# Performance work log

Measured on AMD Instinct MI355X. Metric: run time of the kernel, lower is better.

The kernel has to match this reference:

```python
import jax, jax.numpy as jnp
import numpy as np

EPS = 1e-5

def _conv1x1(x, w):
    # x: (B, Cin, N, K), w: (Cout, Cin) -> (B, Cout, N, K)
    return jnp.einsum('oc,bcnk->bonk', w, x)

def _bn2d(x, gamma, beta):
    # eval-mode BN with running_mean=0, running_var=1 (fresh init)
    scale = gamma / jnp.sqrt(1.0 + EPS)
    return x * scale[None, :, None, None] + beta[None, :, None, None]

def setup_inputs() -> dict:
    key = jax.random.key(0)
    ks = jax.random.split(key, 10)
    B, Cin, N, K = 8, 64, 1024, 32
    Cout, M = 64, 8
    Cin2 = 2 * Cin  # kernel_input='w_neighbor'
    features = jax.random.normal(ks[0], (B, Cin, N, K), dtype=jnp.float32)
    points_xyz = jax.random.normal(ks[1], (B, 3, N, K), dtype=jnp.float32)
    # ScoreNet convs: mlp_channels [7,16,16,16,M]; first 3 have BN (no bias), last has bias
    w1 = jax.random.normal(ks[2], (16, 7), dtype=jnp.float32) * (2.0 / 7) ** 0.5
    w2 = jax.random.normal(ks[3], (16, 16), dtype=jnp.float32) * (2.0 / 16) ** 0.5
    w3 = jax.random.normal(ks[4], (16, 16), dtype=jnp.float32) * (2.0 / 16) ** 0.5
    w4 = jax.random.normal(ks[5], (M, 16), dtype=jnp.float32) * (2.0 / 16) ** 0.5
    b4 = jnp.zeros((M,), dtype=jnp.float32)
    g1 = jnp.ones((16,), jnp.float32); be1 = jnp.zeros((16,), jnp.float32)
    g2 = jnp.ones((16,), jnp.float32); be2 = jnp.zeros((16,), jnp.float32)
    g3 = jnp.ones((16,), jnp.float32); be3 = jnp.zeros((16,), jnp.float32)
    # weight bank: kaiming_normal on (M, 2Cin, Cout) -> stored as (2Cin, M, Cout)
    wb = jax.random.normal(ks[6], (Cin2, M, Cout), dtype=jnp.float32) * (2.0 / Cin2) ** 0.5
    bn_g = jnp.ones((Cout,), jnp.float32); bn_b = jnp.zeros((Cout,), jnp.float32)
    return dict(features=features, points_xyz=points_xyz,
                w1=w1, g1=g1, be1=be1, w2=w2, g2=g2, be2=be2,
                w3=w3, g3=g3, be3=be3, w4=w4, b4=b4,
                weight_bank=wb, bn_g=bn_g, bn_b=bn_b)

def reference(features, points_xyz, w1, g1, be1, w2, g2, be2, w3, g3, be3,
              w4, b4, weight_bank, bn_g, bn_b):
    B, Cin, N, K = features.shape
    M = weight_bank.shape[1]
    # kernel_input = 'w_neighbor': concat(feat - center, feat) -> (B, 2Cin, N, K)
    center_f = features[..., :1]
    feat = jnp.concatenate([features - center_f, features], axis=1)
    # scorenet input = 'w_neighbor_dist': (center_xyz, xyz_diff, dist) -> (B, 7, N, K)
    center_xyz = jnp.broadcast_to(points_xyz[..., :1], points_xyz.shape)
    xyz_diff = points_xyz - center_xyz
    dist = jnp.sqrt(jnp.sum(xyz_diff * xyz_diff, axis=1, keepdims=True))
    xyz_feats = jnp.concatenate([center_xyz, xyz_diff, dist], axis=1)
    h = jax.nn.relu(_bn2d(_conv1x1(xyz_feats, w1), g1, be1))
    h = jax.nn.relu(_bn2d(_conv1x1(h, w2), g2, be2))
    h = jax.nn.relu(_bn2d(_conv1x1(h, w3), g3, be3))
    s = _conv1x1(h, w4) + b4[None, :, None, None]  # (B, M, N, K)
    scores = jax.nn.softmax(s, axis=1)
    scores = jnp.transpose(scores, (0, 2, 3, 1))  # (B, N, K, M)
    # matmul with weight bank then score-weighted sum over kernels, fused via einsum
    # original: (B,N,K,2Cin)@(2Cin,M*Cout) -> (B,N,K,M,Cout); sum_m scores * . -> (B,N,K,Cout)
    new_features = jnp.einsum('bcnk,cmo,bnkm->bonk', feat, weight_bank, scores)
    # BN2d (eval, fresh stats) + ReLU
    new_features = jax.nn.relu(_bn2d(new_features, bn_g, bn_b))
    return new_features
```

## Files before the change

kernel.cpp:

```cpp
#include <hip/hip_runtime.h>
#include <hip/hip_bf16.h>

typedef _Float16 f16;
typedef __attribute__((ext_vector_type(2))) _Float16 f16x2;
typedef __attribute__((ext_vector_type(8))) _Float16 f16x8;
typedef __attribute__((ext_vector_type(16))) float f32x16;

#define BNSCL 0.9999950000375f

__global__ __launch_bounds__(256) void k_scores(
    const float* __restrict__ xyz,
    const float* __restrict__ w1, const float* __restrict__ g1, const float* __restrict__ be1,
    const float* __restrict__ w2, const float* __restrict__ g2, const float* __restrict__ be2,
    const float* __restrict__ w3, const float* __restrict__ g3, const float* __restrict__ be3,
    const float* __restrict__ w4, const float* __restrict__ b4,
    const float* __restrict__ wb, f16* __restrict__ wbtA,
    f16* __restrict__ scores)
{
    __shared__ float lw[856];
    const int tid = threadIdx.x;

    if (blockIdx.x < 256) {
        int idx = blockIdx.x * 256 + tid;
        int j    = idx & 7;
        int lane = (idx >> 3) & 63;
        int ks   = (idx >> 9) & 63;
        int ot   = idx >> 15;
        int cp   = ks * 2 + (lane >> 5);
        int o    = ot * 32 + (lane & 31);
        wbtA[idx] = (f16)wb[(cp * 8 + j) * 64 + o];
    }

    if (tid < 112) lw[tid] = w1[tid];
    lw[112 + tid] = w2[tid];
    lw[368 + tid] = w3[tid];
    if (tid < 128) lw[624 + tid] = w4[tid];
    if (tid < 8)   lw[752 + tid] = b4[tid];
    if (tid < 16) {
        lw[760 + tid] = g1[tid] * BNSCL;  lw[776 + tid] = be1[tid];
        lw[792 + tid] = g2[tid] * BNSCL;  lw[808 + tid] = be2[tid];
        lw[824 + tid] = g3[tid] * BNSCL;  lw[840 + tid] = be3[tid];
    }
    __syncthreads();

    float in7[2][7], h1[2][16], h2[2][16], s[2][8];

#pragma unroll
    for (int q = 0; q < 2; ++q) {
        int g = blockIdx.x * 512 + q * 256 + tid;
        int b = g >> 15;
        int p = g & 32767;
        int pc = p & ~31;
        const float* xb = xyz + (size_t)b * 98304;
        float cx = xb[pc], cy = xb[32768 + pc], cz = xb[65536 + pc];
        float dx = xb[p] - cx, dy = xb[32768 + p] - cy, dz = xb[65536 + p] - cz;
        in7[q][0] = cx; in7[q][1] = cy; in7[q][2] = cz;
        in7[q][3] = dx; in7[q][4] = dy; in7[q][5] = dz;
        in7[q][6] = sqrtf(dx * dx + dy * dy + dz * dz);
    }

#pragma unroll
    for (int o = 0; o < 16; ++o) {
        float a0 = 0.f, a1 = 0.f;
#pragma unroll
        for (int c = 0; c < 7; ++c) {
            float w = lw[o * 7 + c];
            a0 += w * in7[0][c]; a1 += w * in7[1][c];
        }
        float gs = lw[760 + o], bb = lw[776 + o];
        h1[0][o] = fmaxf(a0 * gs + bb, 0.f);
        h1[1][o] = fmaxf(a1 * gs + bb, 0.f);
    }
#pragma unroll
    for (int o = 0; o < 16; ++o) {
        float a0 = 0.f, a1 = 0.f;
#pragma unroll
        for (int c = 0; c < 16; ++c) {
            float w = lw[112 + o * 16 + c];
            a0 += w * h1[0][c]; a1 += w * h1[1][c];
        }
        float gs = lw[792 + o], bb = lw[808 + o];
        h2[0][o] = fmaxf(a0 * gs + bb, 0.f);
        h2[1][o] = fmaxf(a1 * gs + bb, 0.f);
    }
#pragma unroll
    for (int o = 0; o < 16; ++o) {
        float a0 = 0.f, a1 = 0.f;
#pragma unroll
        for (int c = 0; c < 16; ++c) {
            float w = lw[368 + o * 16 + c];
            a0 += w * h2[0][c]; a1 += w * h2[1][c];
        }
        float gs = lw[824 + o], bb = lw[840 + o];
        h1[0][o] = fmaxf(a0 * gs + bb, 0.f);
        h1[1][o] = fmaxf(a1 * gs + bb, 0.f);
    }
#pragma unroll
    for (int o = 0; o < 8; ++o) {
        float bb = lw[752 + o];
        float a0 = bb, a1 = bb;
#pragma unroll
        for (int c = 0; c < 16; ++c) {
            float w = lw[624 + o * 16 + c];
            a0 += w * h1[0][c]; a1 += w * h1[1][c];
        }
        s[0][o] = a0; s[1][o] = a1;
    }

#pragma unroll
    for (int q = 0; q < 2; ++q) {
        int g = blockIdx.x * 512 + q * 256 + tid;
        float mx = s[q][0];
#pragma unroll
        for (int i = 1; i < 8; ++i) mx = fmaxf(mx, s[q][i]);
        float sum = 0.f;
#pragma unroll
        for (int i = 0; i < 8; ++i) { s[q][i] = __expf(s[q][i] - mx); sum += s[q][i]; }
        float inv = 1.f / sum;
        f16x8 o8;
#pragma unroll
        for (int i = 0; i < 8; ++i) o8[i] = (f16)(s[q][i] * inv);
        *(f16x8*)(scores + (size_t)g * 8) = o8;
    }
}

__global__ __launch_bounds__(256, 3) void k_main(
    const float* __restrict__ feat,
    const f16* __restrict__ scores,
    const f16* __restrict__ wbtA,
    const float* __restrict__ bn_g, const float* __restrict__ bn_b,
    float* __restrict__ out)
{
    const int tid  = threadIdx.x;
    const int lane = tid & 63;
    const int wave = tid >> 6;
    const int l31  = lane & 31;
    const int lh   = lane >> 5;

    const int pblock = blockIdx.x * 256;
    const int b    = pblock >> 15;
    const int pt0  = (pblock & 32767) + wave * 64;
    const int pc0  = pt0 + l31;
    const int pc1  = pc0 + 32;

    const float* fb = feat + (size_t)b * 2097152;

    const int gpt = pblock + wave * 64 + l31;
    f16x8 sv0 = *(const f16x8*)(scores + (size_t)gpt * 8);
    f16x8 sv1 = *(const f16x8*)(scores + (size_t)(gpt + 32) * 8);
    const f16x2 s0a = {sv0[0], sv0[1]}, s0b = {sv0[2], sv0[3]},
                s0c = {sv0[4], sv0[5]}, s0d = {sv0[6], sv0[7]};
    const f16x2 s1a = {sv1[0], sv1[1]}, s1b = {sv1[2], sv1[3]},
                s1c = {sv1[4], sv1[5]}, s1d = {sv1[6], sv1[7]};

    f32x16 acc00 = {}, acc01 = {}, acc10 = {}, acc11 = {};

    const f16* A = wbtA + (lane << 3);

#pragma unroll 2
    for (int kk = 0; kk < 32; ++kk) {
        const float* fr = fb + ((size_t)(kk * 2 + lh) << 15);

        f16x8 aD0 = *(const f16x8*)(A + ((size_t)(0 * 64 + kk)       << 9));
        f16x8 aD1 = *(const f16x8*)(A + ((size_t)(1 * 64 + kk)       << 9));
        f16x8 aR0 = *(const f16x8*)(A + ((size_t)(0 * 64 + kk + 32)  << 9));
        f16x8 aR1 = *(const f16x8*)(A + ((size_t)(1 * 64 + kk + 32)  << 9));

        float fv0 = fr[pc0], fv1 = fr[pc1];
        float fc0 = fr[pt0], fc1 = fr[pt0 + 32];

        f16 hR0 = (f16)fv0,          hR1 = (f16)fv1;
        f16 hD0 = (f16)(fv0 - fc0),  hD1 = (f16)(fv1 - fc1);
        f16x2 fR0 = {hR0, hR0}, fR1 = {hR1, hR1};
        f16x2 fD0 = {hD0, hD0}, fD1 = {hD1, hD1};

        f16x2 d0a = fD0 * s0a, d0b = fD0 * s0b, d0c = fD0 * s0c, d0d = fD0 * s0d;
        f16x2 d1a = fD1 * s1a, d1b = fD1 * s1b, d1c = fD1 * s1c, d1d = fD1 * s1d;
        f16x2 r0a = fR0 * s0a, r0b = fR0 * s0b, r0c = fR0 * s0c, r0d = fR0 * s0d;
        f16x2 r1a = fR1 * s1a, r1b = fR1 * s1b, r1c = fR1 * s1c, r1d = fR1 * s1d;

        f16x8 bD0 = {d0a[0],d0a[1],d0b[0],d0b[1],d0c[0],d0c[1],d0d[0],d0d[1]};
        f16x8 bD1 = {d1a[0],d1a[1],d1b[0],d1b[1],d1c[0],d1c[1],d1d[0],d1d[1]};
        f16x8 bR0 = {r0a[0],r0a[1],r0b[0],r0b[1],r0c[0],r0c[1],r0d[0],r0d[1]};
        f16x8 bR1 = {r1a[0],r1a[1],r1b[0],r1b[1],r1c[0],r1c[1],r1d[0],r1d[1]};

        acc00 = __builtin_amdgcn_mfma_f32_32x32x16_f16(aD0, bD0, acc00, 0, 0, 0);
        acc01 = __builtin_amdgcn_mfma_f32_32x32x16_f16(aD1, bD0, acc01, 0, 0, 0);
        acc10 = __builtin_amdgcn_mfma_f32_32x32x16_f16(aD0, bD1, acc10, 0, 0, 0);
        acc11 = __builtin_amdgcn_mfma_f32_32x32x16_f16(aD1, bD1, acc11, 0, 0, 0);
        acc00 = __builtin_amdgcn_mfma_f32_32x32x16_f16(aR0, bR0, acc00, 0, 0, 0);
        acc01 = __builtin_amdgcn_mfma_f32_32x32x16_f16(aR1, bR0, acc01, 0, 0, 0);
        acc10 = __builtin_amdgcn_mfma_f32_32x32x16_f16(aR0, bR1, acc10, 0, 0, 0);
        acc11 = __builtin_amdgcn_mfma_f32_32x32x16_f16(aR1, bR1, acc11, 0, 0, 0);
    }

#pragma unroll
    for (int q = 0; q < 2; ++q) {
        int pcol = (q == 0) ? pc0 : pc1;
#pragma unroll
        for (int ot = 0; ot < 2; ++ot) {
            const f32x16& a = (q == 0) ? (ot == 0 ? acc00 : acc01)
                                       : (ot == 0 ? acc10 : acc11);
#pragma unroll
            for (int r = 0; r < 16; ++r) {
                int o = ot * 32 + (r & 3) + ((r >> 2) << 3) + (lh << 2);
                float v = a[r];
                v = v * (bn_g[o] * BNSCL) + bn_b[o];
                v = fmaxf(v, 0.f);
                out[((size_t)(b * 64 + o) << 15) + pcol] = v;
            }
        }
    }
}

extern "C" void kernel_launch(void* const* d_in, const int* in_sizes, int n_in,
                              void* d_out, int out_size, void* d_ws, size_t ws_size,
                              hipStream_t stream)
{
    const float* features = (const float*)d_in[0];
    const float* xyz      = (const float*)d_in[1];
    const float* w1  = (const float*)d_in[2];
    const float* g1  = (const float*)d_in[3];
    const float* be1 = (const float*)d_in[4];
    const float* w2  = (const float*)d_in[5];
    const float* g2  = (const float*)d_in[6];
    const float* be2 = (const float*)d_in[7];
    const float* w3  = (const float*)d_in[8];
    const float* g3  = (const float*)d_in[9];
    const float* be3 = (const float*)d_in[10];
    const float* w4  = (const float*)d_in[11];
    const float* b4  = (const float*)d_in[12];
    const float* wb  = (const float*)d_in[13];
    const float* bn_g = (const float*)d_in[14];
    const float* bn_b = (const float*)d_in[15];

    f16* scores = (f16*)d_ws;
    f16* wbtA   = (f16*)((char*)d_ws + (4u << 20));

    k_scores<<<512, 256, 0, stream>>>(xyz, w1, g1, be1, w2, g2, be2,
                                      w3, g3, be3, w4, b4, wb, wbtA, scores);
    k_main<<<1024, 256, 0, stream>>>(features, scores, wbtA, bn_g, bn_b,
                                     (float*)d_out);
}
```

Measured before the change: 189.0 us.

## Split output channels across blocks and stage weight-bank tile in LDS

Each block now handles one 32-wide output-channel half for 512 points (8 waves) and copies its 64KB weight-bank slice into shared memory once, reading A fragments from LDS instead of global memory. Accumulators drop from four to two per wave, which cuts register pressure and allows higher occupancy. In exchange, the features and scores are read twice (once per output half), and the 64KB LDS allocation plus the staging barrier limit how many blocks fit per CU.

New measurement: 180.3 us. 4.6% less time.

```diff
diff --git a/kernel.cpp b/kernel.cpp
--- a/kernel.cpp
+++ b/kernel.cpp
@@ -124,24 +124,36 @@
     }
 }
 
-__global__ __launch_bounds__(256, 3) void k_main(
+__global__ __launch_bounds__(512, 4) void k_main(
     const float* __restrict__ feat,
     const f16* __restrict__ scores,
     const f16* __restrict__ wbtA,
     const float* __restrict__ bn_g, const float* __restrict__ bn_b,
     float* __restrict__ out)
 {
+    __shared__ __align__(16) f16 lwb[32768];
+
     const int tid  = threadIdx.x;
     const int lane = tid & 63;
     const int wave = tid >> 6;
     const int l31  = lane & 31;
     const int lh   = lane >> 5;
 
-    const int pblock = blockIdx.x * 256;
+    const int ot = blockIdx.x >> 9;
+    const int g  = blockIdx.x & 511;
+    const int pblock = g * 512;
     const int b    = pblock >> 15;
     const int pt0  = (pblock & 32767) + wave * 64;
     const int pc0  = pt0 + l31;
     const int pc1  = pc0 + 32;
+
+    const f16* src = wbtA + ((size_t)ot << 15);
+#pragma unroll
+    for (int it = 0; it < 8; ++it) {
+        int idx = it * 512 + tid;
+        *(int4*)&lwb[idx << 3] = *(const int4*)&src[idx << 3];
+    }
+    __syncthreads();
 
     const float* fb = feat + (size_t)b * 2097152;
 
@@ -153,18 +165,16 @@
     const f16x2 s1a = {sv1[0], sv1[1]}, s1b = {sv1[2], sv1[3]},
                 s1c = {sv1[4], sv1[5]}, s1d = {sv1[6], sv1[7]};
 
-    f32x16 acc00 = {}, acc01 = {}, acc10 = {}, acc11 = {};
-
-    const f16* A = wbtA + (lane << 3);
+    f32x16 acc0 = {}, acc1 = {};
+
+    const f16* Alds = lwb + (lane << 3);
 
 #pragma unroll 2
     for (int kk = 0; kk < 32; ++kk) {
         const float* fr = fb + ((size_t)(kk * 2 + lh) << 15);
 
-        f16x8 aD0 = *(const f16x8*)(A + ((size_t)(0 * 64 + kk)       << 9));
-        f16x8 aD1 = *(const f16x8*)(A + ((size_t)(1 * 64 + kk)       << 9));
-        f16x8 aR0 = *(const f16x8*)(A + ((size_t)(0 * 64 + kk + 32)  << 9));
-        f16x8 aR1 = *(const f16x8*)(A + ((size_t)(1 * 64 + kk + 32)  << 9));
+        f16x8 aD = *(const f16x8*)(Alds + ((size_t)kk << 9));
+        f16x8 aR = *(const f16x8*)(Alds + ((size_t)(kk + 32) << 9));
 
         float fv0 = fr[pc0], fv1 = fr[pc1];
         float fc0 = fr[pt0], fc1 = fr[pt0 + 32];
@@ -184,31 +194,23 @@
         f16x8 bR0 = {r0a[0],r0a[1],r0b[0],r0b[1],r0c[0],r0c[1],r0d[0],r0d[1]};
         f16x8 bR1 = {r1a[0],r1a[1],r1b[0],r1b[1],r1c[0],r1c[1],r1d[0],r1d[1]};
 
-        acc00 = __builtin_amdgcn_mfma_f32_32x32x16_f16(aD0, bD0, acc00, 0, 0, 0);
-        acc01 = __builtin_amdgcn_mfma_f32_32x32x16_f16(aD1, bD0, acc01, 0, 0, 0);
-        acc10 = __builtin_amdgcn_mfma_f32_32x32x16_f16(aD0, bD1, acc10, 0, 0, 0);
-        acc11 = __builtin_amdgcn_mfma_f32_32x32x16_f16(aD1, bD1, acc11, 0, 0, 0);
-        acc00 = __builtin_amdgcn_mfma_f32_32x32x16_f16(aR0, bR0, acc00, 0, 0, 0);
-        acc01 = __builtin_amdgcn_mfma_f32_32x32x16_f16(aR1, bR0, acc01, 0, 0, 0);
-        acc10 = __builtin_amdgcn_mfma_f32_32x32x16_f16(aR0, bR1, acc10, 0, 0, 0);
-        acc11 = __builtin_amdgcn_mfma_f32_32x32x16_f16(aR1, bR1, acc11, 0, 0, 0);
+        acc0 = __builtin_amdgcn_mfma_f32_32x32x16_f16(aD, bD0, acc0, 0, 0, 0);
+        acc1 = __builtin_amdgcn_mfma_f32_32x32x16_f16(aD, bD1, acc1, 0, 0, 0);
+        acc0 = __builtin_amdgcn_mfma_f32_32x32x16_f16(aR, bR0, acc0, 0, 0, 0);
+        acc1 = __builtin_amdgcn_mfma_f32_32x32x16_f16(aR, bR1, acc1, 0, 0, 0);
     }
 
 #pragma unroll
     for (int q = 0; q < 2; ++q) {
         int pcol = (q == 0) ? pc0 : pc1;
-#pragma unroll
-        for (int ot = 0; ot < 2; ++ot) {
-            const f32x16& a = (q == 0) ? (ot == 0 ? acc00 : acc01)
-                                       : (ot == 0 ? acc10 : acc11);
-#pragma unroll
-            for (int r = 0; r < 16; ++r) {
-                int o = ot * 32 + (r & 3) + ((r >> 2) << 3) + (lh << 2);
-                float v = a[r];
-                v = v * (bn_g[o] * BNSCL) + bn_b[o];
-                v = fmaxf(v, 0.f);
-                out[((size_t)(b * 64 + o) << 15) + pcol] = v;
-            }
+        const f32x16& a = (q == 0) ? acc0 : acc1;
+#pragma unroll
+        for (int r = 0; r < 16; ++r) {
+            int o = ot * 32 + (r & 3) + ((r >> 2) << 3) + (lh << 2);
+            float v = a[r];
+            v = v * (bn_g[o] * BNSCL) + bn_b[o];
+            v = fmaxf(v, 0.f);
+            out[((size_t)(b * 64 + o) << 15) + pcol] = v;
         }
     }
 }
@@ -239,6 +241,6 @@
 
     k_scores<<<512, 256, 0, stream>>>(xyz, w1, g1, be1, w2, g2, be2,
                                       w3, g3, be3, w4, b4, wb, wbtA, scores);
-    k_main<<<1024, 256, 0, stream>>>(features, scores, wbtA, bn_g, bn_b,
+    k_main<<<1024, 512, 0, stream>>>(features, scores, wbtA, bn_g, bn_b,
                                      (float*)d_out);
 }
```
